# Kernel tuning notes

Hardware: AMD Instinct MI355X
Metric: run time of the kernel (lower is better)

The kernel has to match this reference:

```python
import jax, jax.numpy as jnp
import numpy as np

D_MODEL = 1024


def setup_inputs() -> dict:
    key = jax.random.key(0)
    ks = jax.random.split(key, 9)
    d = D_MODEL
    s = 1.0 / np.sqrt(d)
    return {
        "x": jax.random.normal(ks[0], (4, 2048, d), dtype=jnp.float32),
        "w_q": jax.random.normal(ks[1], (d, d), dtype=jnp.float32) * s,
        "b_q": jnp.zeros((d,), dtype=jnp.float32),
        "w_k": jax.random.normal(ks[2], (d, d), dtype=jnp.float32) * s,
        "b_k": jnp.zeros((d,), dtype=jnp.float32),
        "w_v": jax.random.normal(ks[3], (d, d), dtype=jnp.float32) * s,
        "b_v": jnp.zeros((d,), dtype=jnp.float32),
        "w_out": jax.random.normal(ks[4], (d, d), dtype=jnp.float32) * s,
        "b_out": jnp.zeros((d,), dtype=jnp.float32),
    }


def reference(x, w_q, b_q, w_k, b_k, w_v, b_v, w_out, b_out):
    d_model = x.shape[-1]
    # torch Linear: y = x @ W^T + b
    Q = jnp.einsum("bsd,ed->bse", x, w_q) + b_q
    K = jnp.einsum("bsd,ed->bse", x, w_k) + b_k
    V = jnp.einsum("bsd,ed->bse", x, w_v) + b_v
    scores = jnp.einsum("bqd,bkd->bqk", Q, K) / jnp.sqrt(jnp.float32(d_model)).astype(x.dtype)
    attn = jax.nn.softmax(scores, axis=-1)
    out = jnp.einsum("bqk,bkd->bqd", attn, V)
    return jnp.einsum("bsd,ed->bse", out, w_out) + b_out
```

## Files before the change

kernel.cpp:

```cpp
#include <hip/hip_runtime.h>


typedef __bf16 bf16x8 __attribute__((ext_vector_type(8)));
typedef float f32x4 __attribute__((ext_vector_type(4)));

__device__ __forceinline__ unsigned short f32_to_bf16(float f) {
  unsigned int u = __float_as_uint(f);
  u += 0x7fffu + ((u >> 16) & 1u);
  return (unsigned short)(u >> 16);
}

__device__ __forceinline__ void load_lds16(const void* g, void* l) {
  __builtin_amdgcn_global_load_lds(
      (const __attribute__((address_space(1))) void*)g,
      (__attribute__((address_space(3))) void*)l, 16, 0, 0);
}

__global__ __launch_bounds__(256) void cast_f32_bf16(
    const float4* __restrict__ in, ushort4* __restrict__ out, int n4) {
  int i = blockIdx.x * 256 + threadIdx.x;
  if (i < n4) {
    float4 f = in[i];
    ushort4 u;
    u.x = f32_to_bf16(f.x);
    u.y = f32_to_bf16(f.y);
    u.z = f32_to_bf16(f.z);
    u.w = f32_to_bf16(f.w);
    out[i] = u;
  }
}

__global__ __launch_bounds__(256) void concat3(
    const float* __restrict__ a, const float* __restrict__ b,
    const float* __restrict__ c, float* __restrict__ o) {
  int i = blockIdx.x * 256 + threadIdx.x;
  if (i < 1024)
    o[i] = a[i];
  else if (i < 2048)
    o[i] = b[i - 1024];
  else if (i < 3072)
    o[i] = c[i - 2048];
}

__global__ __launch_bounds__(512, 2) void gemm_bt256dp(
    const unsigned short* __restrict__ A, const unsigned short* __restrict__ B,
    void* __restrict__ C, const float* __restrict__ bias,
    int M, int N, int K, float alpha, int out_bf16, int lda, int ldb,
    long long sA, long long sB, long long sC) {
  __shared__ unsigned short As[3][2][128 * 64];
  __shared__ unsigned short Bs[2][2][128 * 64];

  const int bz = blockIdx.z;
  A += (long long)bz * sA;
  B += (long long)bz * sB;

  const int bm = blockIdx.y, bn = blockIdx.x;
  const int tid = threadIdx.x;
  const int lane = tid & 63, wave = tid >> 6;
  const int wr = wave >> 2;
  const int wc = wave & 3;
  const int l16 = lane & 15, quad = lane >> 4;
  const int wbh = wc >> 1;
  const int wbr = (wc & 1) * 64 + l16;
  const int pc0 = (quad ^ (l16 & 7)) * 8;
  const int pc1 = ((4 + quad) ^ (l16 & 7)) * 8;

  const int srow = tid >> 3;
  const int lch = (tid & 7) ^ (srow & 7);
  const unsigned short* gA0 = A + (long long)(bm * 256 + srow) * lda + lch * 8;
  const unsigned short* gB0 = B + (long long)(bn * 256 + srow) * ldb + lch * 8;

  f32x4 acc[8][4] = {};
  bf16x8 af[2][2];
  bf16x8 bf[4][2];

  const int NT = K >> 6;

#define STA(BUF, H, KT)                                                     \
  do {                                                                      \
    const unsigned short* _s =                                              \
        gA0 + (long long)(H) * 128 * lda + (long long)(KT) * 64;            \
    char* _d = (char*)&As[BUF][H][0] + wave * 1024;                         \
    load_lds16(_s, _d);                                                     \
    load_lds16(_s + (long long)64 * lda, _d + 8192);                        \
  } while (0)
#define STB(BUF, H, KT)                                                     \
  do {                                                                      \
    const unsigned short* _s =                                              \
        gB0 + (long long)(H) * 128 * ldb + (long long)(KT) * 64;            \
    char* _d = (char*)&Bs[BUF][H][0] + wave * 1024;                         \
    load_lds16(_s, _d);                                                     \
    load_lds16(_s + (long long)64 * ldb, _d + 8192);                        \
  } while (0)

#define DSAq(BUF, MIP)                                                      \
  do {                                                                      \
    _Pragma("unroll") for (int m2 = 0; m2 < 2; ++m2) {                      \
      const unsigned short* _r =                                            \
          &As[BUF][wr][(((MIP) * 2 + m2) * 16 + l16) * 64];                 \
      af[m2][0] = *(const bf16x8*)(_r + pc0);                               \
      af[m2][1] = *(const bf16x8*)(_r + pc1);                               \
    }                                                                       \
  } while (0)

#define DSBq(BUF)                                                           \
  do {                                                                      \
    _Pragma("unroll") for (int ni = 0; ni < 4; ++ni) {                      \
      const unsigned short* _r = &Bs[BUF][wbh][(wbr + ni * 16) * 64];       \
      bf[ni][0] = *(const bf16x8*)(_r + pc0);                               \
      bf[ni][1] = *(const bf16x8*)(_r + pc1);                               \
    }                                                                       \
  } while (0)

#define MMq(MIP)                                                            \
  do {                                                                      \
    _Pragma("unroll") for (int m2 = 0; m2 < 2; ++m2)                        \
        _Pragma("unroll") for (int ni = 0; ni < 4; ++ni) {                  \
      f32x4* _a = &acc[(MIP) * 2 + m2][ni];                                 \
      *_a = __builtin_amdgcn_mfma_f32_16x16x32_bf16(af[m2][0], bf[ni][0],   \
                                                    *_a, 0, 0, 0);          \
      *_a = __builtin_amdgcn_mfma_f32_16x16x32_bf16(af[m2][1], bf[ni][1],   \
                                                    *_a, 0, 0, 0);          \
    }                                                                       \
  } while (0)

#define BARx() __builtin_amdgcn_s_barrier()
#define WLGx() asm volatile("s_waitcnt lgkmcnt(0)" ::: "memory")
#define WVM8() asm volatile("s_waitcnt vmcnt(8)" ::: "memory")
#define PR1() __builtin_amdgcn_s_setprio(1)
#define PR0() __builtin_amdgcn_s_setprio(0)

  STA(0, 0, 0);
  STA(0, 1, 0);
  STB(0, 0, 0);
  STB(0, 1, 0);
  STA(1, 0, 1);
  STA(1, 1, 1);
  STB(1, 0, 1);
  STB(1, 1, 1);
  WVM8();
  BARx();

  int a = 0;
  for (int t = 0; t < NT; ++t) {
    const int b = t & 1;
    int a2 = a + 2;
    if (a2 >= 3) a2 -= 3;
    const int kt2 = (t + 2 < NT) ? t + 2 : NT - 1;
    DSBq(b);
    DSAq(a, 0);
    STA(a2, 0, kt2);
    BARx();
    WLGx();
    PR1();
    MMq(0);
    PR0();
    BARx();
    DSAq(a, 1);
    STA(a2, 1, kt2);
    BARx();
    WLGx();
    PR1();
    MMq(1);
    PR0();
    BARx();
    DSAq(a, 2);
    STB(b, 0, kt2);
    BARx();
    WLGx();
    PR1();
    MMq(2);
    PR0();
    BARx();
    DSAq(a, 3);
    STB(b, 1, kt2);
    BARx();
    WLGx();
    PR1();
    MMq(3);
    PR0();
    WVM8();
    BARx();
    ++a;
    if (a == 3) a = 0;
  }
  asm volatile("s_waitcnt vmcnt(0)" ::: "memory");

  const long long orow0 = (long long)bm * 256 + wr * 128 + quad * 4;
  const int ocol0 = bn * 256 + wc * 64 + l16;
  if (out_bf16) {
    unsigned short* Cp = (unsigned short*)C + (long long)bz * sC;
#pragma unroll
    for (int mi = 0; mi < 8; ++mi)
#pragma unroll
      for (int ni = 0; ni < 4; ++ni) {
        const int col = ocol0 + ni * 16;
        const float bv = bias ? bias[col] : 0.f;
#pragma unroll
        for (int r = 0; r < 4; ++r) {
          const float o = acc[mi][ni][r] * alpha + bv;
          Cp[(orow0 + mi * 16 + r) * N + col] = f32_to_bf16(o);
        }
      }
  } else {
    float* Cp = (float*)C + (long long)bz * sC;
#pragma unroll
    for (int mi = 0; mi < 8; ++mi)
#pragma unroll
      for (int ni = 0; ni < 4; ++ni) {
        const int col = ocol0 + ni * 16;
        const float bv = bias ? bias[col] : 0.f;
#pragma unroll
        for (int r = 0; r < 4; ++r) {
          const float o = acc[mi][ni][r] * alpha + bv;
          Cp[(orow0 + mi * 16 + r) * N + col] = o;
        }
      }
  }
#undef STA
#undef STB
#undef DSAq
#undef DSBq
#undef MMq
#undef BARx
#undef WLGx
#undef WVM8
#undef PR1
#undef PR0
}

__global__ __launch_bounds__(512, 2) void gemm_bt128x256(
    const unsigned short* __restrict__ A, const unsigned short* __restrict__ B,
    void* __restrict__ C, const float* __restrict__ bias,
    int M, int N, int K, float alpha, int out_bf16, int lda, int ldb,
    long long sA, long long sB, long long sC) {
  __shared__ unsigned short As[3][128][64];
  __shared__ unsigned short Bs[3][256][64];

  const int bz = blockIdx.z;
  A += (long long)bz * sA;
  B += (long long)bz * sB;

  const int bm = blockIdx.y, bn = blockIdx.x;
  const int tid = threadIdx.x;
  const int lane = tid & 63, wave = tid >> 6;
  const int wr = wave >> 2;
  const int wc = wave & 3;
  const int l16 = lane & 15, quad = lane >> 4;
  const int pc0 = (quad ^ (l16 & 7)) * 8;
  const int pc1 = ((4 + quad) ^ (l16 & 7)) * 8;

  const int srow = tid >> 3;
  const int lch = (tid & 7) ^ (srow & 7);
  const unsigned short* gA0 = A + (long long)(bm * 128 + srow) * lda + lch * 8;
  const unsigned short* gB0 = B + (long long)(bn * 256 + srow) * ldb + lch * 8;

  f32x4 acc[4][4] = {};
  bf16x8 af[2][2];
  bf16x8 bf[4][2];

  const int NT = K >> 6;

#define STG_A(BUF, KT)                                                      \
  do {                                                                      \
    const unsigned short* _s = gA0 + (long long)(KT) * 64;                  \
    char* _d = (char*)&As[BUF][0][0] + wave * 1024;                         \
    load_lds16(_s, _d);                                                     \
    load_lds16(_s + (long long)64 * lda, _d + 8192);                        \
  } while (0)
#define STG_B(BUF, KT, J0, JN)                                              \
  do {                                                                      \
    const unsigned short* _s = gB0 + (long long)(KT) * 64;                  \
    char* _d = (char*)&Bs[BUF][0][0] + wave * 1024;                         \
    _Pragma("unroll") for (int _j = (J0); _j < (JN); ++_j)                  \
        load_lds16(_s + (long long)(_j * 64) * ldb, _d + _j * 8192);        \
  } while (0)

#define DSA(BUF, P)                                                         \
  do {                                                                      \
    _Pragma("unroll") for (int m2 = 0; m2 < 2; ++m2) {                      \
      const unsigned short* _r =                                            \
          &As[BUF][wr * 64 + ((P) * 2 + m2) * 16 + l16][0];                 \
      af[m2][0] = *(const bf16x8*)(_r + pc0);                               \
      af[m2][1] = *(const bf16x8*)(_r + pc1);                               \
    }                                                                       \
  } while (0)

#define DSB(BUF)                                                            \
  do {                                                                      \
    _Pragma("unroll") for (int ni = 0; ni < 4; ++ni) {                      \
      const unsigned short* _r = &Bs[BUF][wc * 64 + ni * 16 + l16][0];      \
      bf[ni][0] = *(const bf16x8*)(_r + pc0);                               \
      bf[ni][1] = *(const bf16x8*)(_r + pc1);                               \
    }                                                                       \
  } while (0)

#define MM(P)                                                               \
  do {                                                                      \
    _Pragma("unroll") for (int m2 = 0; m2 < 2; ++m2)                        \
        _Pragma("unroll") for (int ni = 0; ni < 4; ++ni) {                  \
      f32x4* _a = &acc[(P) * 2 + m2][ni];                                   \
      *_a = __builtin_amdgcn_mfma_f32_16x16x32_bf16(af[m2][0], bf[ni][0],   \
                                                    *_a, 0, 0, 0);          \
      *_a = __builtin_amdgcn_mfma_f32_16x16x32_bf16(af[m2][1], bf[ni][1],   \
                                                    *_a, 0, 0, 0);          \
    }                                                                       \
  } while (0)

#define BAR() __builtin_amdgcn_s_barrier()
#define WLG() asm volatile("s_waitcnt lgkmcnt(0)" ::: "memory")
#define WVM6() asm volatile("s_waitcnt vmcnt(6)" ::: "memory")
#define P1x() __builtin_amdgcn_s_setprio(1)
#define P0x() __builtin_amdgcn_s_setprio(0)

  STG_A(0, 0);
  STG_B(0, 0, 0, 4);
  STG_A(1, 1);
  STG_B(1, 1, 0, 4);
  WVM6();
  BAR();

  int cur = 0;
  for (int t = 0; t < NT; ++t) {
    int b2 = cur + 2;
    if (b2 >= 3) b2 -= 3;
    const int kt = (t + 2 < NT) ? t + 2 : NT - 1;
    DSB(cur);
    DSA(cur, 0);
    STG_A(b2, kt);
    STG_B(b2, kt, 0, 1);
    BAR();
    WLG();
    P1x();
    MM(0);
    P0x();
    BAR();
    DSA(cur, 1);
    STG_B(b2, kt, 1, 4);
    BAR();
    WLG();
    P1x();
    MM(1);
    P0x();
    WVM6();
    BAR();
    ++cur;
    if (cur == 3) cur = 0;
  }
  asm volatile("s_waitcnt vmcnt(0)" ::: "memory");

  const long long orow0 = (long long)bm * 128 + wr * 64 + quad * 4;
  const int ocol0 = bn * 256 + wc * 64 + l16;
  if (out_bf16) {
    unsigned short* Cp = (unsigned short*)C + (long long)bz * sC;
#pragma unroll
    for (int mi = 0; mi < 4; ++mi)
#pragma unroll
      for (int ni = 0; ni < 4; ++ni) {
        const int col = ocol0 + ni * 16;
        const float bv = bias ? bias[col] : 0.f;
#pragma unroll
        for (int r = 0; r < 4; ++r) {
          const float o = acc[mi][ni][r] * alpha + bv;
          Cp[(orow0 + mi * 16 + r) * N + col] = f32_to_bf16(o);
        }
      }
  } else {
    float* Cp = (float*)C + (long long)bz * sC;
#pragma unroll
    for (int mi = 0; mi < 4; ++mi)
#pragma unroll
      for (int ni = 0; ni < 4; ++ni) {
        const int col = ocol0 + ni * 16;
        const float bv = bias ? bias[col] : 0.f;
#pragma unroll
        for (int r = 0; r < 4; ++r) {
          const float o = acc[mi][ni][r] * alpha + bv;
          Cp[(orow0 + mi * 16 + r) * N + col] = o;
        }
      }
  }
#undef STG_A
#undef STG_B
#undef DSA
#undef DSB
#undef MM
#undef BAR
#undef WLG
#undef WVM6
#undef P1x
#undef P0x
}

__global__ __launch_bounds__(256) void transpose_v(
    const unsigned short* __restrict__ V, unsigned short* __restrict__ VT,
    int ldv) {
  __shared__ unsigned short tile[64][65];
  const int d0 = blockIdx.x * 64, s0 = blockIdx.y * 64, b = blockIdx.z;
  const int t = threadIdx.x;
  const unsigned short* src = V + ((long long)b * 2048 + s0) * ldv + d0;
#pragma unroll
  for (int i = 0; i < 16; i++) {
    int lin = t + i * 256;
    int r = lin >> 6, c = lin & 63;
    tile[r][c] = src[(long long)r * ldv + c];
  }
  __syncthreads();
  unsigned short* dst = VT + ((long long)b * 1024 + d0) * 2048 + s0;
#pragma unroll
  for (int i = 0; i < 16; i++) {
    int lin = t + i * 256;
    int r = lin >> 6, c = lin & 63;
    dst[(long long)r * 2048 + c] = tile[c][r];
  }
}

__global__ __launch_bounds__(256) void softmax_rows(
    const float* __restrict__ S, unsigned short* __restrict__ P) {
  const long long row = blockIdx.x;
  const float* s = S + row * 2048;
  const int t = threadIdx.x;
  float v[8];
  float mx = -3.4e38f;
#pragma unroll
  for (int i = 0; i < 8; i++) {
    v[i] = s[t + i * 256];
    mx = fmaxf(mx, v[i]);
  }
#pragma unroll
  for (int o = 32; o >= 1; o >>= 1) mx = fmaxf(mx, __shfl_xor(mx, o));
  __shared__ float red[4], red2[4];
  if ((t & 63) == 0) red[t >> 6] = mx;
  __syncthreads();
  mx = fmaxf(fmaxf(red[0], red[1]), fmaxf(red[2], red[3]));
  float sum = 0.f;
#pragma unroll
  for (int i = 0; i < 8; i++) {
    v[i] = __expf(v[i] - mx);
    sum += v[i];
  }
#pragma unroll
  for (int o = 32; o >= 1; o >>= 1) sum += __shfl_xor(sum, o);
  if ((t & 63) == 0) red2[t >> 6] = sum;
  __syncthreads();
  sum = red2[0] + red2[1] + red2[2] + red2[3];
  const float inv = 1.0f / sum;
  unsigned short* p = P + row * 2048;
#pragma unroll
  for (int i = 0; i < 8; i++) p[t + i * 256] = f32_to_bf16(v[i] * inv);
}

extern "C" void kernel_launch(void* const* d_in, const int* in_sizes, int n_in,
                              void* d_out, int out_size, void* d_ws,
                              size_t ws_size, hipStream_t stream) {
  const float* x = (const float*)d_in[0];
  const float* wq = (const float*)d_in[1];
  const float* bq = (const float*)d_in[2];
  const float* wk = (const float*)d_in[3];
  const float* bk = (const float*)d_in[4];
  const float* wv = (const float*)d_in[5];
  const float* bv = (const float*)d_in[6];
  const float* wo = (const float*)d_in[7];
  const float* bo = (const float*)d_in[8];
  float* out = (float*)d_out;
  char* ws = (char*)d_ws;
  const size_t MB = 1ull << 20;

  unsigned short* xb   = (unsigned short*)(ws + 0);
  unsigned short* wqkv = (unsigned short*)(ws + 16 * MB);
  unsigned short* wkb  = (unsigned short*)(ws + 18 * MB);
  unsigned short* wvb  = (unsigned short*)(ws + 20 * MB);
  unsigned short* wob  = (unsigned short*)(ws + 22 * MB);
  unsigned short* QKV  = (unsigned short*)(ws + 24 * MB);
  float*          S    = (float*)(ws + 72 * MB);
  float*          bqkv = (float*)(ws + 72 * MB);
  unsigned short* VT   = xb;
  unsigned short* P    = QKV;
  unsigned short* O    = (unsigned short*)(ws + 56 * MB);

  cast_f32_bf16<<<dim3(8192), dim3(256), 0, stream>>>((const float4*)x,
                                                      (ushort4*)xb, 2097152);
  cast_f32_bf16<<<dim3(1024), dim3(256), 0, stream>>>((const float4*)wq,
                                                      (ushort4*)wqkv, 262144);
  cast_f32_bf16<<<dim3(1024), dim3(256), 0, stream>>>((const float4*)wk,
                                                      (ushort4*)wkb, 262144);
  cast_f32_bf16<<<dim3(1024), dim3(256), 0, stream>>>((const float4*)wv,
                                                      (ushort4*)wvb, 262144);
  cast_f32_bf16<<<dim3(1024), dim3(256), 0, stream>>>((const float4*)wo,
                                                      (ushort4*)wob, 262144);
  concat3<<<dim3(12), dim3(256), 0, stream>>>(bq, bk, bv, bqkv);

  gemm_bt256dp<<<dim3(12, 32, 1), dim3(512), 0, stream>>>(
      xb, wqkv, QKV, bqkv, 8192, 3072, 1024, 1.f, 1, 1024, 1024, 0, 0, 0);

  transpose_v<<<dim3(16, 32, 4), dim3(256), 0, stream>>>(QKV + 2048, VT, 3072);

  gemm_bt256dp<<<dim3(8, 8, 4), dim3(512), 0, stream>>>(
      QKV, QKV + 1024, S, nullptr, 2048, 2048, 1024, 0.03125f, 0, 3072, 3072,
      2048ll * 3072, 2048ll * 3072, 2048ll * 2048);

  softmax_rows<<<dim3(8192), dim3(256), 0, stream>>>(S, P);

  gemm_bt128x256<<<dim3(4, 16, 4), dim3(512), 0, stream>>>(
      P, VT, O, nullptr, 2048, 1024, 2048, 1.f, 1, 2048, 2048, 2048ll * 2048,
      1024ll * 2048, 2048ll * 1024);

  gemm_bt128x256<<<dim3(4, 64, 1), dim3(512), 0, stream>>>(
      O, wob, out, bo, 8192, 1024, 1024, 1.f, 0, 1024, 1024, 0, 0, 0);
}
```

Baseline: 314.3 us.

## Compute V transposed via GEMM, fuse cast kernels, add XCD-aware block remap

The five cast launches and the bias concat become one prep kernel. V is no longer produced by the QKV GEMM and then transposed. Instead a separate GEMM computes W_v·x^T directly into the V^T layout, using a new row-bias option, and the QK projection shrinks to N=2048. Both GEMM kernels now remap linear block IDs so consecutive tiles land on the same XCD, which should improve L2 reuse. The price is an extra GEMM launch in place of the transpose and some index arithmetic per block.

After: 297.5 us. -5.3%, faster.

```diff
diff --git a/kernel.cpp b/kernel.cpp
--- a/kernel.cpp
+++ b/kernel.cpp
@@ -10,36 +10,49 @@
   return (unsigned short)(u >> 16);
 }
 
+__device__ __forceinline__ ushort4 cvt4(float4 f) {
+  ushort4 u;
+  u.x = f32_to_bf16(f.x);
+  u.y = f32_to_bf16(f.y);
+  u.z = f32_to_bf16(f.z);
+  u.w = f32_to_bf16(f.w);
+  return u;
+}
+
 __device__ __forceinline__ void load_lds16(const void* g, void* l) {
   __builtin_amdgcn_global_load_lds(
       (const __attribute__((address_space(1))) void*)g,
       (__attribute__((address_space(3))) void*)l, 16, 0, 0);
 }
 
-__global__ __launch_bounds__(256) void cast_f32_bf16(
-    const float4* __restrict__ in, ushort4* __restrict__ out, int n4) {
+__global__ __launch_bounds__(256) void prep(
+    const float4* __restrict__ x, const float4* __restrict__ wq,
+    const float4* __restrict__ wk, const float4* __restrict__ wv,
+    const float4* __restrict__ wo, const float4* __restrict__ bq,
+    const float4* __restrict__ bk, ushort4* __restrict__ xb,
+    ushort4* __restrict__ wqk, ushort4* __restrict__ wvb,
+    ushort4* __restrict__ wob, float4* __restrict__ bqk) {
+  const int NX = 2097152;
+  const int NW = 262144;
   int i = blockIdx.x * 256 + threadIdx.x;
-  if (i < n4) {
-    float4 f = in[i];
-    ushort4 u;
-    u.x = f32_to_bf16(f.x);
-    u.y = f32_to_bf16(f.y);
-    u.z = f32_to_bf16(f.z);
-    u.w = f32_to_bf16(f.w);
-    out[i] = u;
-  }
-}
-
-__global__ __launch_bounds__(256) void concat3(
-    const float* __restrict__ a, const float* __restrict__ b,
-    const float* __restrict__ c, float* __restrict__ o) {
-  int i = blockIdx.x * 256 + threadIdx.x;
-  if (i < 1024)
-    o[i] = a[i];
-  else if (i < 2048)
-    o[i] = b[i - 1024];
-  else if (i < 3072)
-    o[i] = c[i - 2048];
+  if (i < NX) {
+    xb[i] = cvt4(x[i]);
+  } else if (i < NX + NW) {
+    int j = i - NX;
+    wqk[j] = cvt4(wq[j]);
+  } else if (i < NX + 2 * NW) {
+    int j = i - NX - NW;
+    wqk[NW + j] = cvt4(wk[j]);
+  } else if (i < NX + 3 * NW) {
+    int j = i - NX - 2 * NW;
+    wvb[j] = cvt4(wv[j]);
+  } else if (i < NX + 4 * NW) {
+    int j = i - NX - 3 * NW;
+    wob[j] = cvt4(wo[j]);
+  } else if (i < NX + 4 * NW + 512) {
+    int j = i - NX - 4 * NW;
+    bqk[j] = (j < 256) ? bq[j] : bk[j - 256];
+  }
 }
 
 __global__ __launch_bounds__(512, 2) void gemm_bt256dp(
@@ -50,11 +63,17 @@
   __shared__ unsigned short As[3][2][128 * 64];
   __shared__ unsigned short Bs[2][2][128 * 64];
 
-  const int bz = blockIdx.z;
+  const int hw = blockIdx.x + gridDim.x * (blockIdx.y + gridDim.y * blockIdx.z);
+  const int nwg = gridDim.x * gridDim.y * gridDim.z;
+  const int lg = (hw & 7) * (nwg >> 3) + (hw >> 3);
+  const int bn = lg % gridDim.x;
+  const int rem = lg / gridDim.x;
+  const int bm = rem % gridDim.y;
+  const int bz = rem / gridDim.y;
+
   A += (long long)bz * sA;
   B += (long long)bz * sB;
 
-  const int bm = blockIdx.y, bn = blockIdx.x;
   const int tid = threadIdx.x;
   const int lane = tid & 63, wave = tid >> 6;
   const int wr = wave >> 2;
@@ -232,16 +251,22 @@
 __global__ __launch_bounds__(512, 2) void gemm_bt128x256(
     const unsigned short* __restrict__ A, const unsigned short* __restrict__ B,
     void* __restrict__ C, const float* __restrict__ bias,
-    int M, int N, int K, float alpha, int out_bf16, int lda, int ldb,
-    long long sA, long long sB, long long sC) {
+    int M, int N, int K, float alpha, int out_bf16, int bias_row,
+    int lda, int ldb, long long sA, long long sB, long long sC) {
   __shared__ unsigned short As[3][128][64];
   __shared__ unsigned short Bs[3][256][64];
 
-  const int bz = blockIdx.z;
+  const int hw = blockIdx.x + gridDim.x * (blockIdx.y + gridDim.y * blockIdx.z);
+  const int nwg = gridDim.x * gridDim.y * gridDim.z;
+  const int lg = (hw & 7) * (nwg >> 3) + (hw >> 3);
+  const int bn = lg % gridDim.x;
+  const int rem = lg / gridDim.x;
+  const int bm = rem % gridDim.y;
+  const int bz = rem / gridDim.y;
+
   A += (long long)bz * sA;
   B += (long long)bz * sB;
 
-  const int bm = blockIdx.y, bn = blockIdx.x;
   const int tid = threadIdx.x;
   const int lane = tid & 63, wave = tid >> 6;
   const int wr = wave >> 2;
@@ -358,9 +383,11 @@
 #pragma unroll
       for (int ni = 0; ni < 4; ++ni) {
         const int col = ocol0 + ni * 16;
-        const float bv = bias ? bias[col] : 0.f;
+        const float bcol = (bias && !bias_row) ? bias[col] : 0.f;
 #pragma unroll
         for (int r = 0; r < 4; ++r) {
+          const float bv =
+              (bias && bias_row) ? bias[orow0 + mi * 16 + r] : bcol;
           const float o = acc[mi][ni][r] * alpha + bv;
           Cp[(orow0 + mi * 16 + r) * N + col] = f32_to_bf16(o);
         }
@@ -372,9 +399,11 @@
 #pragma unroll
       for (int ni = 0; ni < 4; ++ni) {
         const int col = ocol0 + ni * 16;
-        const float bv = bias ? bias[col] : 0.f;
+        const float bcol = (bias && !bias_row) ? bias[col] : 0.f;
 #pragma unroll
         for (int r = 0; r < 4; ++r) {
+          const float bv =
+              (bias && bias_row) ? bias[orow0 + mi * 16 + r] : bcol;
           const float o = acc[mi][ni][r] * alpha + bv;
           Cp[(orow0 + mi * 16 + r) * N + col] = o;
         }
@@ -390,29 +419,6 @@
 #undef WVM6
 #undef P1x
 #undef P0x
-}
-
-__global__ __launch_bounds__(256) void transpose_v(
-    const unsigned short* __restrict__ V, unsigned short* __restrict__ VT,
-    int ldv) {
-  __shared__ unsigned short tile[64][65];
-  const int d0 = blockIdx.x * 64, s0 = blockIdx.y * 64, b = blockIdx.z;
-  const int t = threadIdx.x;
-  const unsigned short* src = V + ((long long)b * 2048 + s0) * ldv + d0;
-#pragma unroll
-  for (int i = 0; i < 16; i++) {
-    int lin = t + i * 256;
-    int r = lin >> 6, c = lin & 63;
-    tile[r][c] = src[(long long)r * ldv + c];
-  }
-  __syncthreads();
-  unsigned short* dst = VT + ((long long)b * 1024 + d0) * 2048 + s0;
-#pragma unroll
-  for (int i = 0; i < 16; i++) {
-    int lin = t + i * 256;
-    int r = lin >> 6, c = lin & 63;
-    dst[(long long)r * 2048 + c] = tile[c][r];
-  }
 }
 
 __global__ __launch_bounds__(256) void softmax_rows(
@@ -466,45 +472,39 @@
   char* ws = (char*)d_ws;
   const size_t MB = 1ull << 20;
 
-  unsigned short* xb   = (unsigned short*)(ws + 0);
-  unsigned short* wqkv = (unsigned short*)(ws + 16 * MB);
-  unsigned short* wkb  = (unsigned short*)(ws + 18 * MB);
-  unsigned short* wvb  = (unsigned short*)(ws + 20 * MB);
-  unsigned short* wob  = (unsigned short*)(ws + 22 * MB);
-  unsigned short* QKV  = (unsigned short*)(ws + 24 * MB);
-  float*          S    = (float*)(ws + 72 * MB);
-  float*          bqkv = (float*)(ws + 72 * MB);
-  unsigned short* VT   = xb;
-  unsigned short* P    = QKV;
-  unsigned short* O    = (unsigned short*)(ws + 56 * MB);
-
-  cast_f32_bf16<<<dim3(8192), dim3(256), 0, stream>>>((const float4*)x,
-                                                      (ushort4*)xb, 2097152);
-  cast_f32_bf16<<<dim3(1024), dim3(256), 0, stream>>>((const float4*)wq,
-                                                      (ushort4*)wqkv, 262144);
-  cast_f32_bf16<<<dim3(1024), dim3(256), 0, stream>>>((const float4*)wk,
-                                                      (ushort4*)wkb, 262144);
-  cast_f32_bf16<<<dim3(1024), dim3(256), 0, stream>>>((const float4*)wv,
-                                                      (ushort4*)wvb, 262144);
-  cast_f32_bf16<<<dim3(1024), dim3(256), 0, stream>>>((const float4*)wo,
-                                                      (ushort4*)wob, 262144);
-  concat3<<<dim3(12), dim3(256), 0, stream>>>(bq, bk, bv, bqkv);
-
-  gemm_bt256dp<<<dim3(12, 32, 1), dim3(512), 0, stream>>>(
-      xb, wqkv, QKV, bqkv, 8192, 3072, 1024, 1.f, 1, 1024, 1024, 0, 0, 0);
-
-  transpose_v<<<dim3(16, 32, 4), dim3(256), 0, stream>>>(QKV + 2048, VT, 3072);
+  unsigned short* xb  = (unsigned short*)(ws + 0);
+  unsigned short* wqk = (unsigned short*)(ws + 16 * MB);
+  unsigned short* wvb = (unsigned short*)(ws + 20 * MB);
+  unsigned short* wob = (unsigned short*)(ws + 22 * MB);
+  unsigned short* QKm = (unsigned short*)(ws + 24 * MB);
+  unsigned short* VT  = (unsigned short*)(ws + 56 * MB);
+  float*          S   = (float*)(ws + 72 * MB);
+  float*          bqk = (float*)(ws + 72 * MB);
+  unsigned short* P   = QKm;
+  unsigned short* O   = xb;
+
+  prep<<<dim3(12290), dim3(256), 0, stream>>>(
+      (const float4*)x, (const float4*)wq, (const float4*)wk,
+      (const float4*)wv, (const float4*)wo, (const float4*)bq,
+      (const float4*)bk, (ushort4*)xb, (ushort4*)wqk, (ushort4*)wvb,
+      (ushort4*)wob, (float4*)bqk);
+
+  gemm_bt256dp<<<dim3(8, 32, 1), dim3(512), 0, stream>>>(
+      xb, wqk, QKm, bqk, 8192, 2048, 1024, 1.f, 1, 1024, 1024, 0, 0, 0);
+
+  gemm_bt128x256<<<dim3(32, 8, 1), dim3(512), 0, stream>>>(
+      wvb, xb, VT, bv, 1024, 8192, 1024, 1.f, 1, 1, 1024, 1024, 0, 0, 0);
 
   gemm_bt256dp<<<dim3(8, 8, 4), dim3(512), 0, stream>>>(
-      QKV, QKV + 1024, S, nullptr, 2048, 2048, 1024, 0.03125f, 0, 3072, 3072,
-      2048ll * 3072, 2048ll * 3072, 2048ll * 2048);
+      QKm, QKm + 1024, S, nullptr, 2048, 2048, 1024, 0.03125f, 0, 2048, 2048,
+      2048ll * 2048, 2048ll * 2048, 2048ll * 2048);
 
   softmax_rows<<<dim3(8192), dim3(256), 0, stream>>>(S, P);
 
   gemm_bt128x256<<<dim3(4, 16, 4), dim3(512), 0, stream>>>(
-      P, VT, O, nullptr, 2048, 1024, 2048, 1.f, 1, 2048, 2048, 2048ll * 2048,
-      1024ll * 2048, 2048ll * 1024);
+      P, VT, O, nullptr, 2048, 1024, 2048, 1.f, 1, 0, 2048, 8192,
+      2048ll * 2048, 2048ll, 2048ll * 1024);
 
   gemm_bt128x256<<<dim3(4, 64, 1), dim3(512), 0, stream>>>(
-      O, wob, out, bo, 8192, 1024, 1024, 1.f, 0, 1024, 1024, 0, 0, 0);
-}
+      O, wob, out, bo, 8192, 1024, 1024, 1.f, 0, 0, 1024, 1024, 0, 0, 0);
+}
```
